# Optimization experiments

Hardware: AMD Instinct MI355X
Metric: run time of the kernel (lower is better)

Reference implementation:

```python
import jax, jax.numpy as jnp
import numpy as np

DIMS = 4

def mlp(x, W1, b1, W2, b2, W3, b3, Wo, bo):
    # x: (4,) -> scalar log(g_rr)
    h = jnp.tanh(x @ W1 + b1)
    h = jnp.tanh(h @ W2 + b2)
    h = jnp.tanh(h @ W3 + b3)
    return (h @ Wo + bo)[0]

def metric(x, params):
    # build_g: spherical metric with learned g_rr = exp(net(x))
    g_rr = jnp.exp(mlp(x, *params))
    r, th = x[1], x[2]
    diag = jnp.stack([-jnp.ones(()), g_rr, r ** 2, (r * jnp.sin(th)) ** 2])
    return jnp.diag(diag)  # (4,4)

def christoffel(x, params):
    g = metric(x, params)
    dg = jax.jacfwd(lambda xx: metric(xx, params))(x)  # dg[i,j,k] = d g_ij / d x^k
    g_inv = jnp.linalg.inv(g)
    # Gamma^a_bc = 0.5 g^{ad} (d_c g_db + d_b g_dc - d_d g_bc)
    sym = dg + jnp.transpose(dg, (0, 2, 1)) - jnp.transpose(dg, (2, 0, 1))
    gamma = 0.5 * jnp.einsum('ad,dbc->abc', g_inv, sym)
    return gamma, g_inv

def einstein_per_sample(x, params):
    gamma, g_inv = christoffel(x, params)
    # D[a,i,j,k] = d_k Gamma^a_ij (second nested forward-mode jacobian)
    D = jax.jacfwd(lambda xx: christoffel(xx, params)[0])(x)
    # R^a_bcd = d_c Gamma^a_db - d_d Gamma^a_cb + G^a_ce G^e_db - G^a_de G^e_cb
    riemann = (jnp.einsum('adbc->abcd', D) - jnp.einsum('acbd->abcd', D)
               + jnp.einsum('ace,edb->abcd', gamma, gamma)
               - jnp.einsum('ade,ecb->abcd', gamma, gamma))
    ricci = jnp.einsum('abad->bd', riemann)
    ricci_scalar = jnp.einsum('bd,bd->', g_inv, ricci)
    ricci_up = jnp.einsum('ac,bd,cd->ab', g_inv, g_inv, ricci)
    return ricci_up - 0.5 * g_inv * ricci_scalar  # contravariant Einstein tensor


def setup_inputs() -> dict:
    key = jax.random.key(0)
    ks = jax.random.split(key, 5)
    B, H = 8192, 256
    # coords in a well-conditioned region (avoid r ~ 0 which makes g singular)
    coords = jax.random.uniform(ks[0], (B, DIMS), dtype=jnp.float32) * 0.9 + 0.1
    def w(k, shape):
        fan_in = shape[0]
        return jax.random.normal(k, shape, dtype=jnp.float32) / np.sqrt(fan_in)
    return {
        'coords': coords,
        'W1': w(ks[1], (DIMS, H)), 'b1': jnp.zeros((H,), jnp.float32),
        'W2': w(ks[2], (H, H)),   'b2': jnp.zeros((H,), jnp.float32),
        'W3': w(ks[3], (H, H)),   'b3': jnp.zeros((H,), jnp.float32),
        'Wo': w(ks[4], (H, 1)),   'bo': jnp.zeros((1,), jnp.float32),
    }


def reference(coords, W1, b1, W2, b2, W3, b3, Wo, bo):
    params = (W1, b1, W2, b2, W3, b3, Wo, bo)
    # Batched Einstein tensor G^{ab}(x) for every sample: (B, 4, 4)
    return jax.vmap(lambda x: einstein_per_sample(x, params))(coords)
```

## Files before the change

kernel.cpp:

```cpp
#include <hip/hip_runtime.h>
#include <math.h>

typedef _Float16 half8 __attribute__((ext_vector_type(8)));
typedef _Float16 half4h __attribute__((ext_vector_type(4)));
typedef float floatx4 __attribute__((ext_vector_type(4)));

#define HDIM 256
#define NC 15
#define NCP 16
#define SPB 8
#define MR 128
#define NWAVE 4
#define NT 4


__device__ __forceinline__ void einstein_tail(
    float f, const float* Gf, const float* Hs, float r, float th,
    float* __restrict__ outp)
{
    const float sn = sinf(th), cs = cosf(th);
    const float E  = expf(f);
    const float r2 = r * r;

    float gi[4];
    gi[0] = -1.f; gi[1] = 1.f / E; gi[2] = 1.f / r2; gi[3] = 1.f / (r2 * sn * sn);

    auto Hfun = [&](int k, int l) -> float {
        int a = k < l ? k : l, b2 = k < l ? l : k;
        int idx = (a == 0) ? b2 : (a == 1) ? 3 + b2 : (a == 2) ? 5 + b2 : 9;
        return Hs[idx];
    };
    auto dgv = [&](int a, int k) -> float {
        if (a == 1) return E * Gf[k];
        if (a == 2) return (k == 1) ? 2.f * r : 0.f;
        if (a == 3) {
            if (k == 1) return 2.f * r * sn * sn;
            if (k == 2) return 2.f * r2 * sn * cs;
        }
        return 0.f;
    };
    auto ddg = [&](int a, int k, int l) -> float {
        if (a == 1) return E * fmaf(Gf[k], Gf[l], Hfun(k, l));
        if (a == 2) return (k == 1 && l == 1) ? 2.f : 0.f;
        if (a == 3) {
            if (k == 1 && l == 1) return 2.f * sn * sn;
            if ((k == 1 && l == 2) || (k == 2 && l == 1)) return 4.f * r * sn * cs;
            if (k == 2 && l == 2) return 2.f * r2 * (cs * cs - sn * sn);
        }
        return 0.f;
    };
    auto SYMF = [&](int a, int i, int jx) -> float {
        float sy = 0.f;
        if (a == i)  sy += dgv(a, jx);
        if (a == jx) sy += dgv(a, i);
        if (i == jx) sy -= dgv(i, a);
        return sy;
    };
    auto DF = [&](int a, int i, int jx, int k) -> float {
        float ds = 0.f;
        if (a == i)  ds += ddg(a, jx, k);
        if (a == jx) ds += ddg(a, i, k);
        if (i == jx) ds -= ddg(i, a, k);
        return 0.5f * (gi[a] * ds - gi[a] * gi[a] * dgv(a, k) * SYMF(a, i, jx));
    };
    auto Gm = [&](int a, int i, int jx) -> float {
        return 0.5f * gi[a] * SYMF(a, i, jx);
    };

    float ric[4][4];
#pragma unroll
    for (int b = 0; b < 4; ++b)
#pragma unroll
        for (int d = 0; d < 4; ++d) {
            float sum = 0.f;
#pragma unroll
            for (int a = 0; a < 4; ++a) {
                sum += DF(a, d, b, a) - DF(a, a, b, d);
#pragma unroll
                for (int e = 0; e < 4; ++e)
                    sum += Gm(a, a, e) * Gm(e, d, b) - Gm(a, d, e) * Gm(e, a, b);
            }
            ric[b][d] = sum;
        }

    float Rs = 0.f;
#pragma unroll
    for (int b = 0; b < 4; ++b) Rs += gi[b] * ric[b][b];

#pragma unroll
    for (int a = 0; a < 4; ++a)
#pragma unroll
        for (int b = 0; b < 4; ++b) {
            float v = gi[a] * gi[b] * ric[a][b];
            if (a == b) v -= 0.5f * gi[a] * Rs;
            outp[a * 4 + b] = v;
        }
}

__global__ __launch_bounds__(1024) void pack_wt(
    const float* __restrict__ W2, const float* __restrict__ W3,
    _Float16* __restrict__ Wt)
{
    __shared__ float t[64][65];
    const int m    = blockIdx.x >> 4;
    const float* W = m ? W3 : W2;
    const int tile = blockIdx.x & 15;
    const int k0 = (tile >> 2) * 64, j0 = (tile & 3) * 64;
    const int tx = threadIdx.x & 63, ty = threadIdx.x >> 6;
#pragma unroll
    for (int i = 0; i < 4; ++i) {
        int k = ty + i * 16;
        t[k][tx] = W[(k0 + k) * HDIM + j0 + tx];
    }
    __syncthreads();
#pragma unroll
    for (int i = 0; i < 4; ++i) {
        int jj = ty + i * 16;
        Wt[(size_t)m * HDIM * HDIM + (j0 + jj) * HDIM + k0 + tx] =
            (_Float16)t[tx][jj];
    }
}

template <bool TW>
__global__ __launch_bounds__(256, 2) void mlp_fused(
    const float* __restrict__ coords,
    const float* __restrict__ W1, const float* __restrict__ b1,
    const float* __restrict__ W2, const float* __restrict__ b2,
    const float* __restrict__ W3, const float* __restrict__ b3,
    const float* __restrict__ Wo, const float* __restrict__ bo,
    const _Float16* __restrict__ Wt,
    float* __restrict__ out, int B)
{
    __shared__ __align__(16) _Float16 st[MR * HDIM];

    const int tid  = threadIdx.x;
    const int w    = tid >> 6;
    const int lane = tid & 63;
    const int col  = lane & 15;
    const int q    = lane >> 4;
    const int s0   = blockIdx.x * SPB;

    floatx4 acc[8][NT];

    auto f4get = [](const float4& v, int i) -> float {
        switch (i & 3) { case 0: return v.x; case 1: return v.y;
                         case 2: return v.z; default: return v.w; }
    };

    auto produce1 = [&]() {
        const int sl = tid & 7;
        const int tc = tid >> 3;
        int ss = s0 + sl; if (ss >= B) ss = B - 1;
        const float x0 = coords[ss * 4 + 0];
        const float x1 = coords[ss * 4 + 1];
        const float x2 = coords[ss * 4 + 2];
        const float x3 = coords[ss * 4 + 3];
        const int jg = tc * 8;
#pragma unroll
        for (int h = 0; h < 2; ++h) {
            float4 wa0 = *(const float4*)&W1[0 * HDIM + jg + 4 * h];
            float4 wa1 = *(const float4*)&W1[1 * HDIM + jg + 4 * h];
            float4 wa2 = *(const float4*)&W1[2 * HDIM + jg + 4 * h];
            float4 wa3 = *(const float4*)&W1[3 * HDIM + jg + 4 * h];
            float4 bb  = *(const float4*)&b1[jg + 4 * h];
            half4h ch4[NCP];
#pragma unroll
            for (int jj = 0; jj < 4; ++jj) ch4[15][jj] = (_Float16)0.f;
#pragma unroll
            for (int jj = 0; jj < 4; ++jj) {
                float w0 = f4get(wa0, jj), w1 = f4get(wa1, jj);
                float w2v = f4get(wa2, jj), w3v = f4get(wa3, jj);
                float a = f4get(bb, jj);
                a = fmaf(x0, w0, a); a = fmaf(x1, w1, a);
                a = fmaf(x2, w2v, a); a = fmaf(x3, w3v, a);
                float v = tanhf(a), tp = 1.f - v * v, m2 = -2.f * v * tp;
                float g[4] = {w0, w1, w2v, w3v};
                ch4[0][jj] = (_Float16)v;
#pragma unroll
                for (int k = 0; k < 4; ++k) ch4[1 + k][jj] = (_Float16)(tp * g[k]);
                int idx = 5;
#pragma unroll
                for (int aa = 0; aa < 4; ++aa)
#pragma unroll
                    for (int bb2 = aa; bb2 < 4; ++bb2) {
                        ch4[idx][jj] = (_Float16)(m2 * g[aa] * g[bb2]); ++idx;
                    }
            }
#pragma unroll
            for (int c = 0; c < NCP; ++c) {
                const int m = 16 * (c >> 1) + 4 * (sl >> 1) + 2 * (sl & 1) + (c & 1);
                const int addr = m * HDIM + (((tc ^ m) & 31) << 3) + 4 * h;
                *(half4h*)&st[addr] = ch4[c];
            }
        }
    };

    auto init_acc = [&](const float* __restrict__ b) {
#pragma unroll
        for (int nt = 0; nt < NT; ++nt) {
            float bj = b[w * 64 + nt * 16 + col];
#pragma unroll
            for (int mt = 0; mt < 8; ++mt)
#pragma unroll
                for (int r = 0; r < 4; ++r) acc[mt][nt][r] = 0.f;
            acc[0][nt][0] = bj;
            acc[0][nt][2] = bj;
        }
    };

    auto gemm_full = [&](const float* __restrict__ W, int layer) {
#pragma unroll
        for (int ks = 0; ks < 8; ++ks) {
            const int kg = ks * 32 + q * 8;
            half8 bf[NT];
#pragma unroll
            for (int nt = 0; nt < NT; ++nt) {
                const int j = w * 64 + nt * 16 + col;
                if constexpr (TW) {
                    bf[nt] = *(const half8*)&Wt[((size_t)layer * HDIM + j) * HDIM + kg];
                } else {
#pragma unroll
                    for (int i = 0; i < 8; ++i)
                        bf[nt][i] = (_Float16)W[(kg + i) * HDIM + j];
                }
            }
            const int lc = ks * 4 + q;
#pragma unroll
            for (int mt = 0; mt < 8; ++mt) {
                const int m = 16 * mt + col;
                half8 af = *(const half8*)&st[m * HDIM + (((lc ^ m) & 31) << 3)];
#pragma unroll
                for (int nt = 0; nt < NT; ++nt)
                    acc[mt][nt] = __builtin_amdgcn_mfma_f32_16x16x32_f16(
                        af, bf[nt], acc[mt][nt], 0, 0, 0);
            }
        }
    };

    auto transform_store = [&]() {
#pragma unroll
        for (int nt = 0; nt < NT; ++nt) {
            const int j = w * 64 + nt * 16 + col;
            const int jc = j >> 3, jb = j & 7;
#pragma unroll
            for (int sv = 0; sv < 2; ++sv) {
                float pre[NCP];
#pragma unroll
                for (int c = 0; c < NCP; ++c)
                    pre[c] = acc[c >> 1][nt][sv * 2 + (c & 1)];
                float v = tanhf(pre[0]), tp = 1.f - v * v, m2 = -2.f * v * tp;
                float g[4] = {pre[1], pre[2], pre[3], pre[4]};
                float ns[NCP];
                ns[0] = v;
#pragma unroll
                for (int k = 0; k < 4; ++k) ns[1 + k] = tp * g[k];
                int idx = 5;
#pragma unroll
                for (int aa = 0; aa < 4; ++aa)
#pragma unroll
                    for (int bb2 = aa; bb2 < 4; ++bb2) {
                        ns[idx] = fmaf(tp, pre[idx], m2 * g[aa] * g[bb2]); ++idx;
                    }
                ns[15] = 0.f;
#pragma unroll
                for (int c = 0; c < NCP; ++c) {
                    const int m = 16 * (c >> 1) + 4 * q + 2 * sv + (c & 1);
                    st[m * HDIM + (((jc ^ m) & 31) << 3) + jb] = (_Float16)ns[c];
                }
            }
        }
    };

    produce1();
    __syncthreads();
    init_acc(b2);
    gemm_full(W2, 0);
    __syncthreads();
    transform_store();
    __syncthreads();
    init_acc(b3);
    gemm_full(W3, 1);

    __syncthreads();
    float* part = (float*)st;
    float* fin  = ((float*)st) + 512;
    float wo[NT];
#pragma unroll
    for (int nt = 0; nt < NT; ++nt) wo[nt] = Wo[w * 64 + nt * 16 + col];

    float on2[2][NC];
#pragma unroll
    for (int sv = 0; sv < 2; ++sv)
#pragma unroll
        for (int c = 0; c < NC; ++c) on2[sv][c] = 0.f;
#pragma unroll
    for (int nt = 0; nt < NT; ++nt)
#pragma unroll
        for (int sv = 0; sv < 2; ++sv) {
            float pre[NCP];
#pragma unroll
            for (int c = 0; c < NCP; ++c)
                pre[c] = acc[c >> 1][nt][sv * 2 + (c & 1)];
            float v = tanhf(pre[0]), tp = 1.f - v * v, m2 = -2.f * v * tp;
            float g[4] = {pre[1], pre[2], pre[3], pre[4]};
            on2[sv][0] = fmaf(wo[nt], v, on2[sv][0]);
#pragma unroll
            for (int k = 0; k < 4; ++k)
                on2[sv][1 + k] = fmaf(wo[nt], tp * g[k], on2[sv][1 + k]);
            int idx = 5;
#pragma unroll
            for (int aa = 0; aa < 4; ++aa)
#pragma unroll
                for (int bb2 = aa; bb2 < 4; ++bb2) {
                    on2[sv][idx] = fmaf(wo[nt],
                        fmaf(tp, pre[idx], m2 * g[aa] * g[bb2]), on2[sv][idx]);
                    ++idx;
                }
        }
#pragma unroll
    for (int mask = 1; mask < 16; mask <<= 1)
#pragma unroll
        for (int sv = 0; sv < 2; ++sv)
#pragma unroll
            for (int c = 0; c < NC; ++c)
                on2[sv][c] += __shfl_xor(on2[sv][c], mask, 64);
    if (col == 0) {
#pragma unroll
        for (int sv = 0; sv < 2; ++sv)
#pragma unroll
            for (int c = 0; c < NC; ++c)
                part[(w * SPB + 2 * q + sv) * NC + c] = on2[sv][c];
    }
    __syncthreads();
    if (tid < SPB * NC) {
        const int sl = tid / NC, c = tid % NC;
        float v = 0.f;
#pragma unroll
        for (int ww = 0; ww < NWAVE; ++ww) v += part[(ww * SPB + sl) * NC + c];
        if (c == 0) v += bo[0];
        fin[sl * 16 + c] = v;
    }
    __syncthreads();
    if (tid < SPB) {
        int s = s0 + tid;
        if (s < B) {
            float f = fin[tid * 16 + 0];
            float Gf[4], Hs[10];
#pragma unroll
            for (int k = 0; k < 4; ++k) Gf[k] = fin[tid * 16 + 1 + k];
#pragma unroll
            for (int qq = 0; qq < 10; ++qq) Hs[qq] = fin[tid * 16 + 5 + qq];
            float r  = coords[s * 4 + 1];
            float th = coords[s * 4 + 2];
            float res[16];
            einstein_tail(f, Gf, Hs, r, th, res);
#pragma unroll
            for (int e = 0; e < 16; ++e) out[s * 16 + e] = res[e];
        }
    }
}

extern "C" void kernel_launch(void* const* d_in, const int* in_sizes, int n_in,
                              void* d_out, int out_size, void* d_ws, size_t ws_size,
                              hipStream_t stream) {
    const float* coords = (const float*)d_in[0];
    const float* W1 = (const float*)d_in[1];
    const float* b1 = (const float*)d_in[2];
    const float* W2 = (const float*)d_in[3];
    const float* b2 = (const float*)d_in[4];
    const float* W3 = (const float*)d_in[5];
    const float* b3 = (const float*)d_in[6];
    const float* Wo = (const float*)d_in[7];
    const float* bo = (const float*)d_in[8];
    float* out = (float*)d_out;
    const int B = in_sizes[0] / 4;
    const int nblocks = (B + SPB - 1) / SPB;

    const size_t wt_bytes = (size_t)2 * HDIM * HDIM * sizeof(_Float16);
    if (ws_size >= wt_bytes) {
        _Float16* Wt = (_Float16*)d_ws;
        pack_wt<<<32, 1024, 0, stream>>>(W2, W3, Wt);
        mlp_fused<true><<<nblocks, 256, 0, stream>>>(
            coords, W1, b1, W2, b2, W3, b3, Wo, bo, Wt, out, B);
    } else {
        mlp_fused<false><<<nblocks, 256, 0, stream>>>(
            coords, W1, b1, W2, b2, W3, b3, Wo, bo, nullptr, out, B);
    }
}
```

Baseline: 132.5 us.

## Halve samples per block and parallelize Einstein tail across 16 lanes

Each block now handles 4 samples instead of 8 (64 instead of 128 M-rows). This halves the accumulator registers, so the launch bound asks for 3 blocks per SM and the grid gets more, smaller blocks. The final Einstein-tensor computation, which used to run serially in one thread per sample, is now spread over 16 lanes per sample. Each lane computes one Ricci component, and the Ricci scalar is formed with a shuffle reduction. The trade-off is that each block amortizes the W2/W3 weight reads over half as many samples, which roughly doubles weight traffic from cache.

```diff
diff --git a/kernel.cpp b/kernel.cpp
--- a/kernel.cpp
+++ b/kernel.cpp
@@ -8,94 +8,11 @@
 #define HDIM 256
 #define NC 15
 #define NCP 16
-#define SPB 8
-#define MR 128
+#define SPB 4
+#define MR 64
 #define NWAVE 4
 #define NT 4
 
-
-__device__ __forceinline__ void einstein_tail(
-    float f, const float* Gf, const float* Hs, float r, float th,
-    float* __restrict__ outp)
-{
-    const float sn = sinf(th), cs = cosf(th);
-    const float E  = expf(f);
-    const float r2 = r * r;
-
-    float gi[4];
-    gi[0] = -1.f; gi[1] = 1.f / E; gi[2] = 1.f / r2; gi[3] = 1.f / (r2 * sn * sn);
-
-    auto Hfun = [&](int k, int l) -> float {
-        int a = k < l ? k : l, b2 = k < l ? l : k;
-        int idx = (a == 0) ? b2 : (a == 1) ? 3 + b2 : (a == 2) ? 5 + b2 : 9;
-        return Hs[idx];
-    };
-    auto dgv = [&](int a, int k) -> float {
-        if (a == 1) return E * Gf[k];
-        if (a == 2) return (k == 1) ? 2.f * r : 0.f;
-        if (a == 3) {
-            if (k == 1) return 2.f * r * sn * sn;
-            if (k == 2) return 2.f * r2 * sn * cs;
-        }
-        return 0.f;
-    };
-    auto ddg = [&](int a, int k, int l) -> float {
-        if (a == 1) return E * fmaf(Gf[k], Gf[l], Hfun(k, l));
-        if (a == 2) return (k == 1 && l == 1) ? 2.f : 0.f;
-        if (a == 3) {
-            if (k == 1 && l == 1) return 2.f * sn * sn;
-            if ((k == 1 && l == 2) || (k == 2 && l == 1)) return 4.f * r * sn * cs;
-            if (k == 2 && l == 2) return 2.f * r2 * (cs * cs - sn * sn);
-        }
-        return 0.f;
-    };
-    auto SYMF = [&](int a, int i, int jx) -> float {
-        float sy = 0.f;
-        if (a == i)  sy += dgv(a, jx);
-        if (a == jx) sy += dgv(a, i);
-        if (i == jx) sy -= dgv(i, a);
-        return sy;
-    };
-    auto DF = [&](int a, int i, int jx, int k) -> float {
-        float ds = 0.f;
-        if (a == i)  ds += ddg(a, jx, k);
-        if (a == jx) ds += ddg(a, i, k);
-        if (i == jx) ds -= ddg(i, a, k);
-        return 0.5f * (gi[a] * ds - gi[a] * gi[a] * dgv(a, k) * SYMF(a, i, jx));
-    };
-    auto Gm = [&](int a, int i, int jx) -> float {
-        return 0.5f * gi[a] * SYMF(a, i, jx);
-    };
-
-    float ric[4][4];
-#pragma unroll
-    for (int b = 0; b < 4; ++b)
-#pragma unroll
-        for (int d = 0; d < 4; ++d) {
-            float sum = 0.f;
-#pragma unroll
-            for (int a = 0; a < 4; ++a) {
-                sum += DF(a, d, b, a) - DF(a, a, b, d);
-#pragma unroll
-                for (int e = 0; e < 4; ++e)
-                    sum += Gm(a, a, e) * Gm(e, d, b) - Gm(a, d, e) * Gm(e, a, b);
-            }
-            ric[b][d] = sum;
-        }
-
-    float Rs = 0.f;
-#pragma unroll
-    for (int b = 0; b < 4; ++b) Rs += gi[b] * ric[b][b];
-
-#pragma unroll
-    for (int a = 0; a < 4; ++a)
-#pragma unroll
-        for (int b = 0; b < 4; ++b) {
-            float v = gi[a] * gi[b] * ric[a][b];
-            if (a == b) v -= 0.5f * gi[a] * Rs;
-            outp[a * 4 + b] = v;
-        }
-}
 
 __global__ __launch_bounds__(1024) void pack_wt(
     const float* __restrict__ W2, const float* __restrict__ W3,
@@ -122,7 +39,7 @@
 }
 
 template <bool TW>
-__global__ __launch_bounds__(256, 2) void mlp_fused(
+__global__ __launch_bounds__(256, 3) void mlp_fused(
     const float* __restrict__ coords,
     const float* __restrict__ W1, const float* __restrict__ b1,
     const float* __restrict__ W2, const float* __restrict__ b2,
@@ -140,7 +57,7 @@
     const int q    = lane >> 4;
     const int s0   = blockIdx.x * SPB;
 
-    floatx4 acc[8][NT];
+    floatx4 acc[4][NT];
 
     auto f4get = [](const float4& v, int i) -> float {
         switch (i & 3) { case 0: return v.x; case 1: return v.y;
@@ -148,50 +65,47 @@
     };
 
     auto produce1 = [&]() {
-        const int sl = tid & 7;
-        const int tc = tid >> 3;
+        const int sl = tid & 3;
+        const int tc = tid >> 2;
         int ss = s0 + sl; if (ss >= B) ss = B - 1;
         const float x0 = coords[ss * 4 + 0];
         const float x1 = coords[ss * 4 + 1];
         const float x2 = coords[ss * 4 + 2];
         const float x3 = coords[ss * 4 + 3];
-        const int jg = tc * 8;
-#pragma unroll
-        for (int h = 0; h < 2; ++h) {
-            float4 wa0 = *(const float4*)&W1[0 * HDIM + jg + 4 * h];
-            float4 wa1 = *(const float4*)&W1[1 * HDIM + jg + 4 * h];
-            float4 wa2 = *(const float4*)&W1[2 * HDIM + jg + 4 * h];
-            float4 wa3 = *(const float4*)&W1[3 * HDIM + jg + 4 * h];
-            float4 bb  = *(const float4*)&b1[jg + 4 * h];
-            half4h ch4[NCP];
-#pragma unroll
-            for (int jj = 0; jj < 4; ++jj) ch4[15][jj] = (_Float16)0.f;
-#pragma unroll
-            for (int jj = 0; jj < 4; ++jj) {
-                float w0 = f4get(wa0, jj), w1 = f4get(wa1, jj);
-                float w2v = f4get(wa2, jj), w3v = f4get(wa3, jj);
-                float a = f4get(bb, jj);
-                a = fmaf(x0, w0, a); a = fmaf(x1, w1, a);
-                a = fmaf(x2, w2v, a); a = fmaf(x3, w3v, a);
-                float v = tanhf(a), tp = 1.f - v * v, m2 = -2.f * v * tp;
-                float g[4] = {w0, w1, w2v, w3v};
-                ch4[0][jj] = (_Float16)v;
-#pragma unroll
-                for (int k = 0; k < 4; ++k) ch4[1 + k][jj] = (_Float16)(tp * g[k]);
-                int idx = 5;
-#pragma unroll
-                for (int aa = 0; aa < 4; ++aa)
-#pragma unroll
-                    for (int bb2 = aa; bb2 < 4; ++bb2) {
-                        ch4[idx][jj] = (_Float16)(m2 * g[aa] * g[bb2]); ++idx;
-                    }
-            }
-#pragma unroll
-            for (int c = 0; c < NCP; ++c) {
-                const int m = 16 * (c >> 1) + 4 * (sl >> 1) + 2 * (sl & 1) + (c & 1);
-                const int addr = m * HDIM + (((tc ^ m) & 31) << 3) + 4 * h;
-                *(half4h*)&st[addr] = ch4[c];
-            }
+        const int jg = tc * 4;
+        float4 wa0 = *(const float4*)&W1[0 * HDIM + jg];
+        float4 wa1 = *(const float4*)&W1[1 * HDIM + jg];
+        float4 wa2 = *(const float4*)&W1[2 * HDIM + jg];
+        float4 wa3 = *(const float4*)&W1[3 * HDIM + jg];
+        float4 bb  = *(const float4*)&b1[jg];
+        half4h ch4[NCP];
+#pragma unroll
+        for (int jj = 0; jj < 4; ++jj) ch4[15][jj] = (_Float16)0.f;
+#pragma unroll
+        for (int jj = 0; jj < 4; ++jj) {
+            float w0 = f4get(wa0, jj), w1 = f4get(wa1, jj);
+            float w2v = f4get(wa2, jj), w3v = f4get(wa3, jj);
+            float a = f4get(bb, jj);
+            a = fmaf(x0, w0, a); a = fmaf(x1, w1, a);
+            a = fmaf(x2, w2v, a); a = fmaf(x3, w3v, a);
+            float v = tanhf(a), tp = 1.f - v * v, m2 = -2.f * v * tp;
+            float g[4] = {w0, w1, w2v, w3v};
+            ch4[0][jj] = (_Float16)v;
+#pragma unroll
+            for (int k = 0; k < 4; ++k) ch4[1 + k][jj] = (_Float16)(tp * g[k]);
+            int idx = 5;
+#pragma unroll
+            for (int aa = 0; aa < 4; ++aa)
+#pragma unroll
+                for (int bb2 = aa; bb2 < 4; ++bb2) {
+                    ch4[idx][jj] = (_Float16)(m2 * g[aa] * g[bb2]); ++idx;
+                }
+        }
+        const int c8 = tc >> 1, o4 = (tc & 1) * 4;
+#pragma unroll
+        for (int c = 0; c < NCP; ++c) {
+            const int m = 16 * (c >> 2) + 4 * sl + (c & 3);
+            *(half4h*)&st[m * HDIM + (((c8 ^ m) & 31) << 3) + o4] = ch4[c];
         }
     };
 
@@ -200,11 +114,10 @@
         for (int nt = 0; nt < NT; ++nt) {
             float bj = b[w * 64 + nt * 16 + col];
 #pragma unroll
-            for (int mt = 0; mt < 8; ++mt)
+            for (int mt = 0; mt < 4; ++mt)
 #pragma unroll
                 for (int r = 0; r < 4; ++r) acc[mt][nt][r] = 0.f;
             acc[0][nt][0] = bj;
-            acc[0][nt][2] = bj;
         }
     };
 
@@ -226,7 +139,7 @@
             }
             const int lc = ks * 4 + q;
 #pragma unroll
-            for (int mt = 0; mt < 8; ++mt) {
+            for (int mt = 0; mt < 4; ++mt) {
                 const int m = 16 * mt + col;
                 half8 af = *(const half8*)&st[m * HDIM + (((lc ^ m) & 31) << 3)];
 #pragma unroll
@@ -242,31 +155,27 @@
         for (int nt = 0; nt < NT; ++nt) {
             const int j = w * 64 + nt * 16 + col;
             const int jc = j >> 3, jb = j & 7;
-#pragma unroll
-            for (int sv = 0; sv < 2; ++sv) {
-                float pre[NCP];
-#pragma unroll
-                for (int c = 0; c < NCP; ++c)
-                    pre[c] = acc[c >> 1][nt][sv * 2 + (c & 1)];
-                float v = tanhf(pre[0]), tp = 1.f - v * v, m2 = -2.f * v * tp;
-                float g[4] = {pre[1], pre[2], pre[3], pre[4]};
-                float ns[NCP];
-                ns[0] = v;
-#pragma unroll
-                for (int k = 0; k < 4; ++k) ns[1 + k] = tp * g[k];
-                int idx = 5;
-#pragma unroll
-                for (int aa = 0; aa < 4; ++aa)
-#pragma unroll
-                    for (int bb2 = aa; bb2 < 4; ++bb2) {
-                        ns[idx] = fmaf(tp, pre[idx], m2 * g[aa] * g[bb2]); ++idx;
-                    }
-                ns[15] = 0.f;
-#pragma unroll
-                for (int c = 0; c < NCP; ++c) {
-                    const int m = 16 * (c >> 1) + 4 * q + 2 * sv + (c & 1);
-                    st[m * HDIM + (((jc ^ m) & 31) << 3) + jb] = (_Float16)ns[c];
-                }
+            float pre[NCP];
+#pragma unroll
+            for (int c = 0; c < NCP; ++c) pre[c] = acc[c >> 2][nt][c & 3];
+            float v = tanhf(pre[0]), tp = 1.f - v * v, m2 = -2.f * v * tp;
+            float g[4] = {pre[1], pre[2], pre[3], pre[4]};
+            float ns[NCP];
+            ns[0] = v;
+#pragma unroll
+            for (int k = 0; k < 4; ++k) ns[1 + k] = tp * g[k];
+            int idx = 5;
+#pragma unroll
+            for (int aa = 0; aa < 4; ++aa)
+#pragma unroll
+                for (int bb2 = aa; bb2 < 4; ++bb2) {
+                    ns[idx] = fmaf(tp, pre[idx], m2 * g[aa] * g[bb2]); ++idx;
+                }
+            ns[15] = 0.f;
+#pragma unroll
+            for (int c = 0; c < NCP; ++c) {
+                const int m = 16 * (c >> 2) + 4 * q + (c & 3);
+                st[m * HDIM + (((jc ^ m) & 31) << 3) + jb] = (_Float16)ns[c];
             }
         }
     };
@@ -283,53 +192,42 @@
 
     __syncthreads();
     float* part = (float*)st;
-    float* fin  = ((float*)st) + 512;
-    float wo[NT];
-#pragma unroll
-    for (int nt = 0; nt < NT; ++nt) wo[nt] = Wo[w * 64 + nt * 16 + col];
-
-    float on2[2][NC];
-#pragma unroll
-    for (int sv = 0; sv < 2; ++sv)
-#pragma unroll
-        for (int c = 0; c < NC; ++c) on2[sv][c] = 0.f;
-#pragma unroll
-    for (int nt = 0; nt < NT; ++nt)
-#pragma unroll
-        for (int sv = 0; sv < 2; ++sv) {
+    float* fin  = ((float*)st) + 256;
+    {
+        float on[NC];
+#pragma unroll
+        for (int c = 0; c < NC; ++c) on[c] = 0.f;
+#pragma unroll
+        for (int nt = 0; nt < NT; ++nt) {
+            const float wo = Wo[w * 64 + nt * 16 + col];
             float pre[NCP];
 #pragma unroll
-            for (int c = 0; c < NCP; ++c)
-                pre[c] = acc[c >> 1][nt][sv * 2 + (c & 1)];
+            for (int c = 0; c < NCP; ++c) pre[c] = acc[c >> 2][nt][c & 3];
             float v = tanhf(pre[0]), tp = 1.f - v * v, m2 = -2.f * v * tp;
             float g[4] = {pre[1], pre[2], pre[3], pre[4]};
-            on2[sv][0] = fmaf(wo[nt], v, on2[sv][0]);
-#pragma unroll
-            for (int k = 0; k < 4; ++k)
-                on2[sv][1 + k] = fmaf(wo[nt], tp * g[k], on2[sv][1 + k]);
+            on[0] = fmaf(wo, v, on[0]);
+#pragma unroll
+            for (int k = 0; k < 4; ++k) on[1 + k] = fmaf(wo, tp * g[k], on[1 + k]);
             int idx = 5;
 #pragma unroll
             for (int aa = 0; aa < 4; ++aa)
 #pragma unroll
                 for (int bb2 = aa; bb2 < 4; ++bb2) {
-                    on2[sv][idx] = fmaf(wo[nt],
-                        fmaf(tp, pre[idx], m2 * g[aa] * g[bb2]), on2[sv][idx]);
+                    on[idx] = fmaf(wo, fmaf(tp, pre[idx], m2 * g[aa] * g[bb2]),
+                                   on[idx]);
                     ++idx;
                 }
         }
 #pragma unroll
-    for (int mask = 1; mask < 16; mask <<= 1)
-#pragma unroll
-        for (int sv = 0; sv < 2; ++sv)
+        for (int mask = 1; mask < 16; mask <<= 1)
 #pragma unroll
             for (int c = 0; c < NC; ++c)
-                on2[sv][c] += __shfl_xor(on2[sv][c], mask, 64);
-    if (col == 0) {
-#pragma unroll
-        for (int sv = 0; sv < 2; ++sv)
+                on[c] += __shfl_xor(on[c], mask, 64);
+        if (col == 0) {
 #pragma unroll
             for (int c = 0; c < NC; ++c)
-                part[(w * SPB + 2 * q + sv) * NC + c] = on2[sv][c];
+                part[(w * SPB + q) * NC + c] = on[c];
+        }
     }
     __syncthreads();
     if (tid < SPB * NC) {
@@ -341,21 +239,95 @@
         fin[sl * 16 + c] = v;
     }
     __syncthreads();
-    if (tid < SPB) {
-        int s = s0 + tid;
+
+    if (tid < 64) {
+        const int sq = tid >> 4;
+        const int e  = tid & 15;
+        const int io = e >> 2, jo = e & 3;
+        const int s  = s0 + sq;
         if (s < B) {
-            float f = fin[tid * 16 + 0];
-            float Gf[4], Hs[10];
-#pragma unroll
-            for (int k = 0; k < 4; ++k) Gf[k] = fin[tid * 16 + 1 + k];
-#pragma unroll
-            for (int qq = 0; qq < 10; ++qq) Hs[qq] = fin[tid * 16 + 5 + qq];
-            float r  = coords[s * 4 + 1];
-            float th = coords[s * 4 + 2];
-            float res[16];
-            einstein_tail(f, Gf, Hs, r, th, res);
-#pragma unroll
-            for (int e = 0; e < 16; ++e) out[s * 16 + e] = res[e];
+            const float f  = fin[sq * 16 + 0];
+            const float G0 = fin[sq * 16 + 1], G1 = fin[sq * 16 + 2];
+            const float G2 = fin[sq * 16 + 3], G3 = fin[sq * 16 + 4];
+            const float h00 = fin[sq * 16 + 5],  h01 = fin[sq * 16 + 6];
+            const float h02 = fin[sq * 16 + 7],  h03 = fin[sq * 16 + 8];
+            const float h11 = fin[sq * 16 + 9],  h12 = fin[sq * 16 + 10];
+            const float h13 = fin[sq * 16 + 11], h22 = fin[sq * 16 + 12];
+            const float h23 = fin[sq * 16 + 13], h33 = fin[sq * 16 + 14];
+            const float r  = coords[s * 4 + 1];
+            const float th = coords[s * 4 + 2];
+            const float sn = sinf(th), cs = cosf(th);
+            const float E  = expf(f);
+            const float r2 = r * r;
+            const float gi1 = 1.f / E, gi2 = 1.f / r2, gi3 = 1.f / (r2 * sn * sn);
+
+            auto GF = [&](int k) -> float {
+                return k == 0 ? G0 : k == 1 ? G1 : k == 2 ? G2 : G3;
+            };
+            auto HS = [&](int k, int l) -> float {
+                int a = k < l ? k : l, b = k < l ? l : k;
+                return a == 0 ? (b == 0 ? h00 : b == 1 ? h01 : b == 2 ? h02 : h03)
+                     : a == 1 ? (b == 1 ? h11 : b == 2 ? h12 : h13)
+                     : a == 2 ? (b == 2 ? h22 : h23) : h33;
+            };
+            auto GI = [&](int a) -> float {
+                return a == 0 ? -1.f : a == 1 ? gi1 : a == 2 ? gi2 : gi3;
+            };
+            auto dgv = [&](int a, int k) -> float {
+                if (a == 1) return E * GF(k);
+                if (a == 2) return k == 1 ? 2.f * r : 0.f;
+                if (a == 3) {
+                    if (k == 1) return 2.f * r * sn * sn;
+                    if (k == 2) return 2.f * r2 * sn * cs;
+                }
+                return 0.f;
+            };
+            auto ddg = [&](int a, int k, int l) -> float {
+                if (a == 1) return E * fmaf(GF(k), GF(l), HS(k, l));
+                if (a == 2) return (k == 1 && l == 1) ? 2.f : 0.f;
+                if (a == 3) {
+                    if (k == 1 && l == 1) return 2.f * sn * sn;
+                    if ((k == 1 && l == 2) || (k == 2 && l == 1))
+                        return 4.f * r * sn * cs;
+                    if (k == 2 && l == 2) return 2.f * r2 * (cs * cs - sn * sn);
+                }
+                return 0.f;
+            };
+            auto SYMF = [&](int a, int i, int jx) -> float {
+                float sy = 0.f;
+                if (a == i)  sy += dgv(a, jx);
+                if (a == jx) sy += dgv(a, i);
+                if (i == jx) sy -= dgv(i, a);
+                return sy;
+            };
+            auto DF = [&](int a, int i, int jx, int k) -> float {
+                float ds = 0.f;
+                if (a == i)  ds += ddg(a, jx, k);
+                if (a == jx) ds += ddg(a, i, k);
+                if (i == jx) ds -= ddg(i, a, k);
+                float ga = GI(a);
+                return 0.5f * (ga * ds - ga * ga * dgv(a, k) * SYMF(a, i, jx));
+            };
+            auto GMf = [&](int a, int i, int jx) -> float {
+                return 0.5f * GI(a) * SYMF(a, i, jx);
+            };
+
+            float ric = 0.f;
+#pragma unroll
+            for (int a = 0; a < 4; ++a) {
+                ric += DF(a, jo, io, a) - DF(a, a, io, jo);
+#pragma unroll
+                for (int ee = 0; ee < 4; ++ee)
+                    ric += GMf(a, a, ee) * GMf(ee, jo, io)
+                         - GMf(a, jo, ee) * GMf(ee, a, io);
+            }
+            float contrib = (io == jo) ? GI(io) * ric : 0.f;
+#pragma unroll
+            for (int mask = 1; mask < 16; mask <<= 1)
+                contrib += __shfl_xor(contrib, mask, 64);
+            float v = GI(io) * GI(jo) * ric;
+            if (io == jo) v -= 0.5f * GI(io) * contrib;
+            out[s * 16 + e] = v;
         }
     }
 }
```

New measurement: 143.8 us. +8.5%, slower.
